# Kernel optimization log

Hardware: AMD Instinct MI355X
Metric: run time of the kernel (lower is better)

## Reference

```python
import jax, jax.numpy as jnp
import numpy as np

DIM = 512
HIDDEN = 1024  # 2.0 * dim
QK = 128
MAX_PEAKS = 256
LN_EPS = 1e-5


def setup_inputs() -> dict:
    key = jax.random.key(0)
    ks = jax.random.split(key, 10)
    b, n = 8, 2048
    x = jax.random.normal(ks[0], (b, n, DIM), dtype=jnp.float32)
    moverz_sin = jax.random.normal(ks[1], (b, n, QK // 2), dtype=jnp.float32)
    moverz_cos = jax.random.normal(ks[2], (b, n, QK // 2), dtype=jnp.float32)
    src_key_padding_mask = jax.random.randint(ks[3], (b, 1, n), 0, 2) > 0
    ln_w = jnp.ones((DIM,), jnp.float32)
    ln_b = jnp.zeros((DIM,), jnp.float32)
    W_hid = jax.random.normal(ks[4], (DIM, 2 * HIDDEN + QK), dtype=jnp.float32) * 0.02
    b_hid = jnp.zeros((2 * HIDDEN + QK,), jnp.float32)
    gamma = jax.random.normal(ks[5], (2, QK), dtype=jnp.float32) * 0.02
    beta = jnp.zeros((2, QK), jnp.float32)
    W_out = jax.random.normal(ks[6], (HIDDEN, DIM), dtype=jnp.float32) * 0.02
    b_out = jnp.zeros((DIM,), jnp.float32)
    return dict(x=x, moverz_sin=moverz_sin, moverz_cos=moverz_cos,
                src_key_padding_mask=src_key_padding_mask,
                ln_w=ln_w, ln_b=ln_b, W_hid=W_hid, b_hid=b_hid,
                gamma=gamma, beta=beta, W_out=W_out, b_out=b_out)


def _apply_moverz(x, sin, cos):
    x0, x1 = x[..., 0::2], x[..., 1::2]
    return jnp.concatenate([x0 * cos - x1 * sin, x1 * cos + x0 * sin], axis=-1)


def reference(x, moverz_sin, moverz_cos, src_key_padding_mask,
              ln_w, ln_b, W_hid, b_hid, gamma, beta, W_out, b_out):
    # LayerNorm + Linear + SiLU
    mu = jnp.mean(x, axis=-1, keepdims=True)
    var = jnp.mean(jnp.square(x - mu), axis=-1, keepdims=True)
    xn = (x - mu) * jax.lax.rsqrt(var + LN_EPS) * ln_w + ln_b
    uv_base = jax.nn.silu(xn @ W_hid + b_hid)  # [b,n,2H+QK]
    u = uv_base[..., :HIDDEN]
    v = uv_base[..., HIDDEN:2 * HIDDEN]
    base = uv_base[..., 2 * HIDDEN:]
    # OffsetScale (heads=2) -> q, k
    q = base * gamma[0] + beta[0]
    k = base * gamma[1] + beta[1]
    q = _apply_moverz(q, moverz_sin, moverz_cos)
    k = _apply_moverz(k, moverz_sin, moverz_cos)
    qk = jnp.einsum('bnr,bmr->bnm', q, k)
    qk = jnp.where(src_key_padding_mask, 0.0, qk)
    attn = jnp.square(jax.nn.relu(qk)) / (MAX_PEAKS * QK)
    out = jnp.einsum('bnm,bmd->bnd', attn, v) * u
    return out @ W_out + b_out + x
```

## Files before the change

### kernel.cpp

```cpp
#include <hip/hip_runtime.h>
#include <hip/hip_bf16.h>
#include <hip/hip_fp8.h>

typedef short short8 __attribute__((ext_vector_type(8)));
typedef float floatx4 __attribute__((ext_vector_type(4)));
typedef int intx8 __attribute__((ext_vector_type(8)));

constexpr int BATCH = 8, SEQ = 2048, DIMC = 512, HID = 1024, QKD = 128, NHID = 2176;
constexpr int TOK = BATCH * SEQ;

constexpr size_t OFF_XN8 = 0;
constexpr size_t OFF_WH8 = OFF_XN8 + (size_t)TOK * DIMC;
constexpr size_t OFF_WO8 = OFF_WH8 + (size_t)NHID * DIMC;
constexpr size_t OFF_U8  = OFF_WO8 + (size_t)DIMC * HID;
constexpr size_t OFF_BSE = OFF_U8  + (size_t)TOK * HID;
constexpr size_t OFF_Q8  = OFF_BSE + (size_t)TOK * QKD * 2;
constexpr size_t OFF_K8  = OFF_Q8  + (size_t)TOK * QKD;
constexpr size_t OFF_VT8 = OFF_K8  + (size_t)TOK * QKD;
constexpr size_t OFF_P8  = OFF_VT8 + (size_t)BATCH * HID * SEQ;
constexpr size_t OFF_HU8 = OFF_P8  + (size_t)BATCH * SEQ * SEQ;

__device__ inline void gload_lds16(const void* g, void* l) {
    __builtin_amdgcn_global_load_lds(
        (const __attribute__((address_space(1))) void*)g,
        (__attribute__((address_space(3))) void*)l, 16, 0, 0);
}

#if __has_builtin(__builtin_amdgcn_cvt_pk_fp8_f32)
__device__ inline int cvtpk8(float a, float b) {
    return __builtin_amdgcn_cvt_pk_fp8_f32(a, b, 0, false);
}
__device__ inline unsigned char f2fp8(float v) {
    return (unsigned char)(cvtpk8(v, v) & 0xff);
}
#else
__device__ inline unsigned char f2fp8(float v) {
    __hip_fp8_e4m3 t(v); return t.__x;
}
__device__ inline int cvtpk8(float a, float b) {
    return (int)f2fp8(a) | ((int)f2fp8(b) << 8);
}
#endif
#if __has_builtin(__builtin_amdgcn_cvt_f32_fp8)
__device__ inline float fp82f(unsigned char b) {
    return __builtin_amdgcn_cvt_f32_fp8((int)b, 0);
}
#else
__device__ inline float fp82f(unsigned char b) {
    __hip_fp8_e4m3 t; t.__x = b; return (float)t;
}
#endif
__device__ inline float fast_rcp(float x) { return __builtin_amdgcn_rcpf(x); }
__device__ inline float fast_silu(float v) { return v * fast_rcp(1.0f + __expf(-v)); }

__global__ __launch_bounds__(256) void ln_kernel(const float* __restrict__ x,
                                                 const float* __restrict__ w,
                                                 const float* __restrict__ b,
                                                 unsigned char* __restrict__ xn8) {
    int t = blockIdx.x;
    const float* xr = x + (size_t)t * DIMC;
    float2 v = ((const float2*)xr)[threadIdx.x];
    float s = v.x + v.y;
    float ss = v.x * v.x + v.y * v.y;
    for (int o = 32; o; o >>= 1) { s += __shfl_down(s, o); ss += __shfl_down(ss, o); }
    __shared__ float red[8];
    int wid = threadIdx.x >> 6, lane = threadIdx.x & 63;
    if (lane == 0) { red[wid] = s; red[4 + wid] = ss; }
    __syncthreads();
    if (threadIdx.x == 0) {
        float a = red[0] + red[1] + red[2] + red[3];
        float q = red[4] + red[5] + red[6] + red[7];
        float mu = a * (1.0f / DIMC);
        red[0] = mu;
        red[4] = q * (1.0f / DIMC) - mu * mu;
    }
    __syncthreads();
    float mu = red[0];
    float inv = rsqrtf(red[4] + 1e-5f);
    int c = threadIdx.x * 2;
    float y0 = (v.x - mu) * inv * w[c] + b[c];
    float y1 = (v.y - mu) * inv * w[c + 1] + b[c + 1];
    int p = cvtpk8(y0, y1);
    uchar2 o2; o2.x = (unsigned char)p; o2.y = (unsigned char)(p >> 8);
    *(uchar2*)&xn8[(size_t)t * DIMC + c] = o2;
}

__global__ __launch_bounds__(256) void cvt_kernel(const float* __restrict__ Wh,
                                                  const float* __restrict__ Wo,
                                                  unsigned char* __restrict__ WhT8,
                                                  unsigned char* __restrict__ WoT8) {
    int i = blockIdx.x * 256 + threadIdx.x;
    const int total1 = NHID * DIMC;
    const int total2 = DIMC * HID;
    if (i < total1) {
        int n = i / DIMC, k = i % DIMC;
        WhT8[i] = f2fp8(Wh[(size_t)k * NHID + n]);
    } else if (i < total1 + total2) {
        int j = i - total1;
        int d = j / HID, h = j % HID;
        WoT8[j] = f2fp8(Wo[(size_t)h * DIMC + d] * 64.0f);
    }
}

__global__ __launch_bounds__(256) void qkrot_kernel(const __hip_bfloat16* __restrict__ bse,
                                                    const float* __restrict__ sn,
                                                    const float* __restrict__ cs,
                                                    const int* __restrict__ mask,
                                                    const float* __restrict__ gamma,
                                                    const float* __restrict__ beta,
                                                    unsigned char* __restrict__ q8,
                                                    unsigned char* __restrict__ k8) {
    int t = blockIdx.x * 4 + (threadIdx.x >> 6);
    int j = threadIdx.x & 63;
    const __hip_bfloat16* base = bse + (size_t)t * QKD;
    float b0 = __bfloat162float(base[2 * j]);
    float b1 = __bfloat162float(base[2 * j + 1]);
    float q0 = b0 * gamma[2 * j] + beta[2 * j];
    float q1 = b1 * gamma[2 * j + 1] + beta[2 * j + 1];
    float k0 = b0 * gamma[QKD + 2 * j] + beta[QKD + 2 * j];
    float k1 = b1 * gamma[QKD + 2 * j + 1] + beta[QKD + 2 * j + 1];
    float s = sn[(size_t)t * 64 + j];
    float c = cs[(size_t)t * 64 + j];
    int bb = t >> 11, nn = t & (SEQ - 1);
    float km = (mask[(size_t)bb * SEQ + nn] != 0) ? 0.f : 16.f;
    int pq = cvtpk8((q0 * c - q1 * s) * 16.f, (q1 * c + q0 * s) * 16.f);
    int pk = cvtpk8((k0 * c - k1 * s) * km, (k1 * c + k0 * s) * km);
    q8[(size_t)t * QKD + j]      = (unsigned char)pq;
    q8[(size_t)t * QKD + 64 + j] = (unsigned char)(pq >> 8);
    k8[(size_t)t * QKD + j]      = (unsigned char)pk;
    k8[(size_t)t * QKD + 64 + j] = (unsigned char)(pk >> 8);
}

template <int EPI, int RAS>
__global__ __launch_bounds__(256, 4) void gemm_mx(
    const unsigned char* __restrict__ A, int lda, long long sA,
    const unsigned char* __restrict__ Bt, int ldb, long long sB,
    int K,
    const float* __restrict__ bias,
    const unsigned char* __restrict__ U8, int ldu, long long sU,
    const float* __restrict__ Xres, int ldx,
    float oscale,
    unsigned char* __restrict__ C8, int ldc8, long long sC8,
    unsigned char* __restrict__ Vt8out,
    __hip_bfloat16* __restrict__ Cbse,
    float* __restrict__ Cf, int ldcf) {
    __shared__ unsigned char As[128 * 128];
    __shared__ unsigned char Bs[128 * 128];

    int m0, n0;
    if (RAS == 0) {
        int lin = blockIdx.x + gridDim.x * blockIdx.y;
        int xcd = lin & 7, j = lin >> 3;
        int gy = gridDim.y;
        m0 = (xcd * (gridDim.x >> 3) + j / gy) * 128;
        n0 = (j % gy) * 128;
    } else {
        int fid = blockIdx.x + gridDim.x * (blockIdx.y + gridDim.y * blockIdx.z);
        int b = fid & 7;
        int r = fid >> 3;
        int gy = gridDim.y;
        n0 = (r % gy) * 128;
        m0 = (r / gy) * 128;
        A += (size_t)b * sA;
        Bt += (size_t)b * sB;
        if (C8) C8 += (size_t)b * sC8;
        if (U8) U8 += (size_t)b * sU;
    }

    int tid = threadIdx.x, lane = tid & 63, wid = tid >> 6;
    int wr = (wid >> 1) * 64, wc = (wid & 1) * 64;
    int r16 = lane & 15, kq = lane >> 4;

    int srow = lane >> 3;
    int sc = (((lane & 7) ^ ((lane >> 3) & 7)) << 4);

    floatx4 acc[4][4] = {};
    const int SCL = 0x7F7F7F7F;

    #define FRGRD(P, row, dst) { \
        uint4* p_ = (uint4*)&(dst); \
        p_[0] = *(const uint4*)&(P)[(row) * 128 + ((((kq * 2)     ^ ((row) & 7))) << 4)]; \
        p_[1] = *(const uint4*)&(P)[(row) * 128 + ((((kq * 2 + 1) ^ ((row) & 7))) << 4)]; }

    for (int kt = 0; kt < K; kt += 128) {
        #pragma unroll
        for (int i = 0; i < 4; i++) {
            int r0 = wid * 32 + i * 8;
            gload_lds16(&A[(size_t)(m0 + r0 + srow) * lda + kt + sc], &As[r0 * 128]);
            gload_lds16(&Bt[(size_t)(n0 + r0 + srow) * ldb + kt + sc], &Bs[r0 * 128]);
        }
        __syncthreads();
        intx8 bfr[4];
        #pragma unroll
        for (int ni = 0; ni < 4; ni++) FRGRD(Bs, wc + ni * 16 + r16, bfr[ni])
        #pragma unroll
        for (int mo = 0; mo < 2; mo++) {
            intx8 afr[2];
            #pragma unroll
            for (int mi = 0; mi < 2; mi++) FRGRD(As, wr + (mo * 2 + mi) * 16 + r16, afr[mi])
            #pragma unroll
            for (int mi = 0; mi < 2; mi++)
                #pragma unroll
                for (int ni = 0; ni < 4; ni++)
                    acc[mo * 2 + mi][ni] = __builtin_amdgcn_mfma_scale_f32_16x16x128_f8f6f4(
                        afr[mi], bfr[ni], acc[mo * 2 + mi][ni], 0, 0, 0, SCL, 0, SCL);
        }
        __syncthreads();
    }
    #undef FRGRD

    #pragma unroll
    for (int mi = 0; mi < 4; mi++) {
        #pragma unroll
        for (int ni = 0; ni < 4; ni++) {
            int rbase = m0 + wr + mi * 16 + kq * 4;
            int col = n0 + wc + ni * 16 + r16;
            if (EPI == 3) {
                #pragma unroll
                for (int i = 0; i < 4; i++) {
                    float v = acc[mi][ni][i] * oscale + bias[col] + Xres[(size_t)(rbase + i) * ldx + col];
                    Cf[(size_t)(rbase + i) * ldcf + col] = v;
                }
            } else {
                float e[4];
                #pragma unroll
                for (int i = 0; i < 4; i++) {
                    float v = acc[mi][ni][i];
                    if (EPI == 0) {
                        v = fast_silu(v + bias[col]);
                    } else if (EPI == 1) {
                        v = v > 0.0f ? v * v * 16.0f : 0.0f;
                    } else {
                        v *= oscale * fp82f(U8[(size_t)(rbase + i) * ldu + col]);
                    }
                    e[i] = v;
                }
                int p01 = cvtpk8(e[0], e[1]);
                int p23 = cvtpk8(e[2], e[3]);
                unsigned char byt[4] = {
                    (unsigned char)p01, (unsigned char)(p01 >> 8),
                    (unsigned char)p23, (unsigned char)(p23 >> 8)};
                if (EPI == 0) {
                    if (n0 < 1024) {
                        #pragma unroll
                        for (int i = 0; i < 4; i++)
                            C8[(size_t)(rbase + i) * HID + col] = byt[i];
                    } else if (n0 < 2048) {
                        uchar4 o; o.x = byt[0]; o.y = byt[1]; o.z = byt[2]; o.w = byt[3];
                        int bb = rbase >> 11, nn = rbase & (SEQ - 1);
                        *(uchar4*)&Vt8out[((size_t)bb * HID + (col - 1024)) * SEQ + nn] = o;
                    } else {
                        #pragma unroll
                        for (int i = 0; i < 4; i++)
                            Cbse[(size_t)(rbase + i) * QKD + col - 2048] = __float2bfloat16(e[i]);
                    }
                } else {
                    #pragma unroll
                    for (int i = 0; i < 4; i++)
                        C8[(size_t)(rbase + i) * ldc8 + col] = byt[i];
                }
            }
        }
    }
}

extern "C" void kernel_launch(void* const* d_in, const int* in_sizes, int n_in,
                              void* d_out, int out_size, void* d_ws, size_t ws_size,
                              hipStream_t stream) {
    const float* x     = (const float*)d_in[0];
    const float* msin  = (const float*)d_in[1];
    const float* mcos  = (const float*)d_in[2];
    const int*   mask  = (const int*)d_in[3];
    const float* lnw   = (const float*)d_in[4];
    const float* lnb   = (const float*)d_in[5];
    const float* Wh    = (const float*)d_in[6];
    const float* bh    = (const float*)d_in[7];
    const float* gamma = (const float*)d_in[8];
    const float* beta  = (const float*)d_in[9];
    const float* Wo    = (const float*)d_in[10];
    const float* bo    = (const float*)d_in[11];
    float* out = (float*)d_out;
    char* ws = (char*)d_ws;

    unsigned char*  xn8  = (unsigned char*)(ws + OFF_XN8);
    unsigned char*  WhT8 = (unsigned char*)(ws + OFF_WH8);
    unsigned char*  WoT8 = (unsigned char*)(ws + OFF_WO8);
    unsigned char*  u8   = (unsigned char*)(ws + OFF_U8);
    __hip_bfloat16* bse  = (__hip_bfloat16*)(ws + OFF_BSE);
    unsigned char*  q8   = (unsigned char*)(ws + OFF_Q8);
    unsigned char*  k8   = (unsigned char*)(ws + OFF_K8);
    unsigned char*  Vt8  = (unsigned char*)(ws + OFF_VT8);
    unsigned char*  P8   = (unsigned char*)(ws + OFF_P8);
    unsigned char*  hu8  = (unsigned char*)(ws + OFF_HU8);

    ln_kernel<<<TOK, 256, 0, stream>>>(x, lnw, lnb, xn8);

    cvt_kernel<<<(NHID * DIMC + DIMC * HID + 255) / 256, 256, 0, stream>>>(Wh, Wo, WhT8, WoT8);

    gemm_mx<0, 0><<<dim3(TOK / 128, NHID / 128), 256, 0, stream>>>(
        xn8, DIMC, 0, WhT8, DIMC, 0, DIMC, bh,
        nullptr, 0, 0, nullptr, 0, 0.0f,
        u8, 0, 0, Vt8, bse, nullptr, 0);

    qkrot_kernel<<<TOK / 4, 256, 0, stream>>>(bse, msin, mcos, mask, gamma, beta, q8, k8);

    gemm_mx<1, 1><<<dim3(SEQ / 128, SEQ / 128, BATCH), 256, 0, stream>>>(
        q8, QKD, (long long)SEQ * QKD, k8, QKD, (long long)SEQ * QKD, QKD, nullptr,
        nullptr, 0, 0, nullptr, 0, 0.0f,
        P8, SEQ, (long long)SEQ * SEQ, nullptr, nullptr, nullptr, 0);

    gemm_mx<2, 1><<<dim3(SEQ / 128, HID / 128, BATCH), 256, 0, stream>>>(
        P8, SEQ, (long long)SEQ * SEQ, Vt8, SEQ, (long long)HID * SEQ, SEQ, nullptr,
        u8, HID, (long long)SEQ * HID, nullptr, 0, 1.9073486328125e-06f ,
        hu8, HID, (long long)SEQ * HID, nullptr, nullptr, nullptr, 0);

    gemm_mx<3, 0><<<dim3(TOK / 128, DIMC / 128), 256, 0, stream>>>(
        hu8, HID, 0, WoT8, HID, 0, HID, bo,
        nullptr, 0, 0, x, DIMC, 2.384185791015625e-07f ,
        nullptr, 0, 0, nullptr, nullptr, out, DIMC);
}
```

Measured before the change: 136.8 us.

## Compact unmasked keys and values to skip masked columns in attention GEMMs

A new per-batch scan kernel computes compacted positions for unmasked keys and the number of 128-wide key tiles in use. K and V^T are written only at those compacted positions. The QK^T GEMM then skips key tiles beyond the count, and the PV GEMM shortens its K loop to match, removing work on masked keys that only ever contributed zeros. The cost is an extra serial scan kernel, index lookups and scattered byte stores in the first GEMM's V epilogue. Padding columns of V^T are left stale, which relies on their matching P entries being exactly zero.

```diff
diff --git a/kernel.cpp b/kernel.cpp
--- a/kernel.cpp
+++ b/kernel.cpp
@@ -15,10 +15,12 @@
 constexpr size_t OFF_U8  = OFF_WO8 + (size_t)DIMC * HID;
 constexpr size_t OFF_BSE = OFF_U8  + (size_t)TOK * HID;
 constexpr size_t OFF_Q8  = OFF_BSE + (size_t)TOK * QKD * 2;
-constexpr size_t OFF_K8  = OFF_Q8  + (size_t)TOK * QKD;
-constexpr size_t OFF_VT8 = OFF_K8  + (size_t)TOK * QKD;
+constexpr size_t OFF_K8C = OFF_Q8  + (size_t)TOK * QKD;
+constexpr size_t OFF_VT8 = OFF_K8C + (size_t)TOK * QKD;
 constexpr size_t OFF_P8  = OFF_VT8 + (size_t)BATCH * HID * SEQ;
 constexpr size_t OFF_HU8 = OFF_P8  + (size_t)BATCH * SEQ * SEQ;
+constexpr size_t OFF_CPS = OFF_HU8 + (size_t)TOK * HID;
+constexpr size_t OFF_NTL = OFF_CPS + (size_t)TOK * 4;
 
 __device__ inline void gload_lds16(const void* g, void* l) {
     __builtin_amdgcn_global_load_lds(
@@ -52,6 +54,43 @@
 #endif
 __device__ inline float fast_rcp(float x) { return __builtin_amdgcn_rcpf(x); }
 __device__ inline float fast_silu(float v) { return v * fast_rcp(1.0f + __expf(-v)); }
+
+__global__ __launch_bounds__(256) void scan_kernel(const int* __restrict__ mask,
+                                                   int* __restrict__ cpos,
+                                                   int* __restrict__ ntl,
+                                                   unsigned char* __restrict__ k8c) {
+    int b = blockIdx.x;
+    __shared__ int sh[256];
+    __shared__ int base;
+    if (threadIdx.x == 0) base = 0;
+    __syncthreads();
+    for (int c = 0; c < 8; c++) {
+        int n = c * 256 + threadIdx.x;
+        int um = (mask[(size_t)b * SEQ + n] == 0) ? 1 : 0;
+        sh[threadIdx.x] = um;
+        __syncthreads();
+        for (int off = 1; off < 256; off <<= 1) {
+            int v = (threadIdx.x >= off) ? sh[threadIdx.x - off] : 0;
+            __syncthreads();
+            sh[threadIdx.x] += v;
+            __syncthreads();
+        }
+        int incl = sh[threadIdx.x];
+        cpos[(size_t)b * SEQ + n] = um ? (base + incl - 1) : -1;
+        __syncthreads();
+        if (threadIdx.x == 255) base += incl;
+        __syncthreads();
+    }
+    int cnt = base;
+    int nt = (cnt + 127) >> 7;
+    if (threadIdx.x == 0) ntl[b] = nt;
+    uint4 z = {0, 0, 0, 0};
+    for (int r = cnt + threadIdx.x; r < nt * 128; r += 256) {
+        uint4* p = (uint4*)&k8c[((size_t)b * SEQ + r) * QKD];
+        #pragma unroll
+        for (int j = 0; j < 8; j++) p[j] = z;
+    }
+}
 
 __global__ __launch_bounds__(256) void ln_kernel(const float* __restrict__ x,
                                                  const float* __restrict__ w,
@@ -105,11 +144,11 @@
 __global__ __launch_bounds__(256) void qkrot_kernel(const __hip_bfloat16* __restrict__ bse,
                                                     const float* __restrict__ sn,
                                                     const float* __restrict__ cs,
-                                                    const int* __restrict__ mask,
+                                                    const int* __restrict__ cpos,
                                                     const float* __restrict__ gamma,
                                                     const float* __restrict__ beta,
                                                     unsigned char* __restrict__ q8,
-                                                    unsigned char* __restrict__ k8) {
+                                                    unsigned char* __restrict__ k8c) {
     int t = blockIdx.x * 4 + (threadIdx.x >> 6);
     int j = threadIdx.x & 63;
     const __hip_bfloat16* base = bse + (size_t)t * QKD;
@@ -121,14 +160,17 @@
     float k1 = b1 * gamma[QKD + 2 * j + 1] + beta[QKD + 2 * j + 1];
     float s = sn[(size_t)t * 64 + j];
     float c = cs[(size_t)t * 64 + j];
-    int bb = t >> 11, nn = t & (SEQ - 1);
-    float km = (mask[(size_t)bb * SEQ + nn] != 0) ? 0.f : 16.f;
     int pq = cvtpk8((q0 * c - q1 * s) * 16.f, (q1 * c + q0 * s) * 16.f);
-    int pk = cvtpk8((k0 * c - k1 * s) * km, (k1 * c + k0 * s) * km);
     q8[(size_t)t * QKD + j]      = (unsigned char)pq;
     q8[(size_t)t * QKD + 64 + j] = (unsigned char)(pq >> 8);
-    k8[(size_t)t * QKD + j]      = (unsigned char)pk;
-    k8[(size_t)t * QKD + 64 + j] = (unsigned char)(pk >> 8);
+    int cp = cpos[t];
+    if (cp >= 0) {
+        int bb = t >> 11;
+        int pk = cvtpk8((k0 * c - k1 * s) * 16.f, (k1 * c + k0 * s) * 16.f);
+        size_t kr = ((size_t)bb * SEQ + cp) * QKD;
+        k8c[kr + j]      = (unsigned char)pk;
+        k8c[kr + 64 + j] = (unsigned char)(pk >> 8);
+    }
 }
 
 template <int EPI, int RAS>
@@ -143,7 +185,8 @@
     unsigned char* __restrict__ C8, int ldc8, long long sC8,
     unsigned char* __restrict__ Vt8out,
     __hip_bfloat16* __restrict__ Cbse,
-    float* __restrict__ Cf, int ldcf) {
+    float* __restrict__ Cf, int ldcf,
+    const int* __restrict__ ntl, const int* __restrict__ cposp) {
     __shared__ unsigned char As[128 * 128];
     __shared__ unsigned char Bs[128 * 128];
 
@@ -165,6 +208,8 @@
         Bt += (size_t)b * sB;
         if (C8) C8 += (size_t)b * sC8;
         if (U8) U8 += (size_t)b * sU;
+        if (EPI == 1 && n0 >= (ntl[b] << 7)) return;
+        if (EPI == 2) K = ntl[b] << 7;
     }
 
     int tid = threadIdx.x, lane = tid & 63, wid = tid >> 6;
@@ -246,9 +291,13 @@
                         for (int i = 0; i < 4; i++)
                             C8[(size_t)(rbase + i) * HID + col] = byt[i];
                     } else if (n0 < 2048) {
-                        uchar4 o; o.x = byt[0]; o.y = byt[1]; o.z = byt[2]; o.w = byt[3];
-                        int bb = rbase >> 11, nn = rbase & (SEQ - 1);
-                        *(uchar4*)&Vt8out[((size_t)bb * HID + (col - 1024)) * SEQ + nn] = o;
+                        int bb = rbase >> 11, nnb = rbase & (SEQ - 1);
+                        #pragma unroll
+                        for (int i = 0; i < 4; i++) {
+                            int cp = cposp[(size_t)bb * SEQ + nnb + i];
+                            if (cp >= 0)
+                                Vt8out[((size_t)bb * HID + (col - 1024)) * SEQ + cp] = byt[i];
+                        }
                     } else {
                         #pragma unroll
                         for (int i = 0; i < 4; i++)
@@ -288,10 +337,14 @@
     unsigned char*  u8   = (unsigned char*)(ws + OFF_U8);
     __hip_bfloat16* bse  = (__hip_bfloat16*)(ws + OFF_BSE);
     unsigned char*  q8   = (unsigned char*)(ws + OFF_Q8);
-    unsigned char*  k8   = (unsigned char*)(ws + OFF_K8);
+    unsigned char*  k8c  = (unsigned char*)(ws + OFF_K8C);
     unsigned char*  Vt8  = (unsigned char*)(ws + OFF_VT8);
     unsigned char*  P8   = (unsigned char*)(ws + OFF_P8);
     unsigned char*  hu8  = (unsigned char*)(ws + OFF_HU8);
+    int*            cpos = (int*)(ws + OFF_CPS);
+    int*            ntl  = (int*)(ws + OFF_NTL);
+
+    scan_kernel<<<BATCH, 256, 0, stream>>>(mask, cpos, ntl, k8c);
 
     ln_kernel<<<TOK, 256, 0, stream>>>(x, lnw, lnb, xn8);
 
@@ -300,22 +353,22 @@
     gemm_mx<0, 0><<<dim3(TOK / 128, NHID / 128), 256, 0, stream>>>(
         xn8, DIMC, 0, WhT8, DIMC, 0, DIMC, bh,
         nullptr, 0, 0, nullptr, 0, 0.0f,
-        u8, 0, 0, Vt8, bse, nullptr, 0);
-
-    qkrot_kernel<<<TOK / 4, 256, 0, stream>>>(bse, msin, mcos, mask, gamma, beta, q8, k8);
+        u8, 0, 0, Vt8, bse, nullptr, 0, nullptr, cpos);
+
+    qkrot_kernel<<<TOK / 4, 256, 0, stream>>>(bse, msin, mcos, cpos, gamma, beta, q8, k8c);
 
     gemm_mx<1, 1><<<dim3(SEQ / 128, SEQ / 128, BATCH), 256, 0, stream>>>(
-        q8, QKD, (long long)SEQ * QKD, k8, QKD, (long long)SEQ * QKD, QKD, nullptr,
+        q8, QKD, (long long)SEQ * QKD, k8c, QKD, (long long)SEQ * QKD, QKD, nullptr,
         nullptr, 0, 0, nullptr, 0, 0.0f,
-        P8, SEQ, (long long)SEQ * SEQ, nullptr, nullptr, nullptr, 0);
+        P8, SEQ, (long long)SEQ * SEQ, nullptr, nullptr, nullptr, 0, ntl, nullptr);
 
     gemm_mx<2, 1><<<dim3(SEQ / 128, HID / 128, BATCH), 256, 0, stream>>>(
         P8, SEQ, (long long)SEQ * SEQ, Vt8, SEQ, (long long)HID * SEQ, SEQ, nullptr,
         u8, HID, (long long)SEQ * HID, nullptr, 0, 1.9073486328125e-06f ,
-        hu8, HID, (long long)SEQ * HID, nullptr, nullptr, nullptr, 0);
+        hu8, HID, (long long)SEQ * HID, nullptr, nullptr, nullptr, 0, ntl, nullptr);
 
     gemm_mx<3, 0><<<dim3(TOK / 128, DIMC / 128), 256, 0, stream>>>(
         hu8, HID, 0, WoT8, HID, 0, HID, bo,
         nullptr, 0, 0, x, DIMC, 2.384185791015625e-07f ,
-        nullptr, 0, 0, nullptr, nullptr, out, DIMC);
-}
+        nullptr, 0, 0, nullptr, nullptr, out, DIMC, nullptr, nullptr);
+}
```

After: 147.4 us. 1.08x slower.
